# Performance work log

Hardware: AMD Instinct MI355X
Metric: run time of the kernel (lower is better)

## Reference

```python
import jax, jax.numpy as jnp
import numpy as np

D_MODEL, D_STATE, V_RANGE, IMG, K = 64, 16, 1, 32, 3
GROUPS = 4
EPS = 1e-5


def _gather_indices():
    H = W = IMG
    v_list = [(x, y) for x in range(-V_RANGE, V_RANGE + 1) for y in range(-V_RANGE, V_RANGE + 1)]
    idx = []
    yg, xg = np.meshgrid(np.arange(H), np.arange(W), indexing='ij')
    for vx, vy in v_list:
        src_y = (yg - vy) % H
        src_x = (xg - vx) % W
        idx.append((src_y * W + src_x).reshape(-1))
    return jnp.asarray(np.stack(idx, axis=0), dtype=jnp.int32)  # (V, H*W)


def setup_inputs() -> dict:
    key = jax.random.key(0)
    ks = jax.random.split(key, 8)
    B = 4
    V = (2 * V_RANGE + 1) ** 2
    fan = D_MODEL * K * K
    std = 1.0 / np.sqrt(fan)
    return {
        'u_t': jax.random.normal(ks[0], (B, D_MODEL, IMG, IMG), jnp.float32),
        's_prev': jax.random.normal(ks[1], (B, V, D_MODEL, D_STATE, IMG, IMG), jnp.float32),
        'gamma': jnp.ones((D_MODEL,), jnp.float32),
        'beta': jnp.zeros((D_MODEL,), jnp.float32),
        'w_delta': jax.random.uniform(ks[2], (D_MODEL, D_MODEL, K, K), jnp.float32, -std, std),
        'b_delta': jax.random.uniform(ks[3], (D_MODEL,), jnp.float32, -std, std),
        'w_B': jax.random.uniform(ks[4], (D_STATE, D_MODEL, K, K), jnp.float32, -std, std),
        'w_C': jax.random.uniform(ks[5], (D_STATE, D_MODEL, K, K), jnp.float32, -std, std),
        'log_A_real': jnp.log(0.5 * jnp.ones((D_MODEL, D_STATE), jnp.float32)),
        'D_param': jnp.ones((D_MODEL,), jnp.float32),
        'dt_inv_softplus': jnp.asarray(np.log(np.exp(1.0) - 1.0), jnp.float32),
        'gather_indices': _gather_indices(),
    }


def _group_norm(x, gamma, beta):
    B, D, H, W = x.shape
    xg = x.reshape(B, GROUPS, D // GROUPS, H, W)
    mu = xg.mean(axis=(2, 3, 4), keepdims=True)
    var = xg.var(axis=(2, 3, 4), keepdims=True)
    xn = ((xg - mu) / jnp.sqrt(var + EPS)).reshape(B, D, H, W)
    return xn * gamma[None, :, None, None] + beta[None, :, None, None]


def _circ_conv(x, w, b=None):
    p = K // 2
    xp = jnp.pad(x, ((0, 0), (0, 0), (p, p), (p, p)), mode='wrap')
    y = jax.lax.conv_general_dilated(xp, w, (1, 1), 'VALID',
                                     dimension_numbers=('NCHW', 'OIHW', 'NCHW'))
    if b is not None:
        y = y + b[None, :, None, None]
    return y


def reference(u_t, s_prev, gamma, beta, w_delta, b_delta, w_B, w_C,
              log_A_real, D_param, dt_inv_softplus, gather_indices):
    B, D, H, W = u_t.shape
    Bv, V, _, N, _, _ = s_prev.shape
    u_norm = _group_norm(u_t, gamma, beta)
    delta = jax.nn.softplus(_circ_conv(u_norm, w_delta, b_delta) + dt_inv_softplus)
    delta = jnp.clip(delta, 1e-4, 5.0)                      # (B,D,H,W)
    B_val = _circ_conv(u_norm, w_B)                          # (B,N,H,W)
    C_val = _circ_conv(u_norm, w_C)                          # (B,N,H,W)
    A = -jnp.exp(log_A_real)                                 # (D,N)
    A_bar = jnp.exp(delta[:, :, None] * A[None, :, :, None, None])  # (B,D,N,H,W)
    B_bar = delta[:, :, None] * B_val[:, None]               # (B,D,N,H,W)
    # flow transport: per-velocity periodic-shift gather over flattened HW
    s_flat = s_prev.reshape(B, V, D, N, H * W)
    s_trans = jax.vmap(lambda sv, iv: jnp.take(sv, iv, axis=-1),
                       in_axes=(1, 0), out_axes=1)(s_flat, gather_indices)
    s_trans = s_trans.reshape(B, V, D, N, H, W)
    s_new = A_bar[:, None] * s_trans + B_bar[:, None] * u_t[:, None, :, None]
    y_state = jnp.sum(s_new * C_val[:, None, None], axis=3)  # (B,V,D,H,W)
    y_new = y_state + u_t[:, None] * D_param[None, None, :, None, None]
    return (y_new, s_new)
```

## Files before the change

### kernel.cpp

```cpp
#include <hip/hip_runtime.h>
#include <hip/hip_bf16.h>

#define D_MODEL 64
#define D_STATE 16
#define IMG     32
#define HW      (IMG*IMG)
#define V       9
#define B       4
#define GROUPS  4
#define CPG     (D_MODEL/GROUPS)

typedef float f32x4 __attribute__((ext_vector_type(4)));

__device__ __forceinline__ void stream_store4(float* p, f32x4 v) {
    asm volatile("global_store_dwordx4 %0, %1, off sc0 sc1 nt"
                 :: "v"(p), "v"(v) : "memory");
}

__global__ __launch_bounds__(256) void gn_kernel(
    const float* __restrict__ u, const float* __restrict__ gamma,
    const float* __restrict__ beta, float* __restrict__ un)
{
    const int b = blockIdx.x / GROUPS;
    const int g = blockIdx.x % GROUPS;
    const float* base = u + ((size_t)b*D_MODEL + g*CPG) * HW;
    const int NE = CPG * HW;

    float s = 0.f, s2 = 0.f;
    for (int i = threadIdx.x; i < NE; i += 256) {
        float v = base[i];
        s += v; s2 += v*v;
    }
    for (int off = 32; off; off >>= 1) {
        s  += __shfl_down(s,  off);
        s2 += __shfl_down(s2, off);
    }
    __shared__ float red0[4], red1[4];
    const int wave = threadIdx.x >> 6;
    if ((threadIdx.x & 63) == 0) { red0[wave] = s; red1[wave] = s2; }
    __syncthreads();
    if (threadIdx.x == 0) {
        float a = 0.f, c = 0.f;
        for (int i = 0; i < 4; i++) { a += red0[i]; c += red1[i]; }
        red0[0] = a; red1[0] = c;
    }
    __syncthreads();
    const float mean = red0[0] * (1.f/16384.f);
    const float var  = red1[0] * (1.f/16384.f) - mean*mean;
    const float rstd = rsqrtf(var + 1e-5f);

    for (int i = threadIdx.x; i < NE; i += 256) {
        int c = i >> 10;
        int d = g*CPG + c;
        float v = (base[i] - mean) * rstd;
        un[((size_t)b*D_MODEL + d)*HW + (i & (HW-1))] = v*gamma[d] + beta[d];
    }
}

__global__ __launch_bounds__(256) void conv_kernel(
    const float* __restrict__ un,
    const float* __restrict__ w_delta, const float* __restrict__ b_delta,
    const float* __restrict__ w_B, const float* __restrict__ w_C,
    const float* __restrict__ dt_sp,
    float* __restrict__ delta, float* __restrict__ Bv, float* __restrict__ Cv)
{
    const int bx    = blockIdx.x;
    const int strip = bx & 3;
    const int cog   = (bx >> 2) % 24;
    const int b     = bx / 96;
    const int co0   = cog * 4;
    const int row0  = strip * 8;

    __shared__ float xs[16][10][32];
    __shared__ float wl[4][D_MODEL*9];

    for (int i = threadIdx.x; i < 4*D_MODEL*9; i += 256) {
        const int cl = i / (D_MODEL*9);
        const int rest = i % (D_MODEL*9);
        const int co = co0 + cl;
        const float* w = (co < 64) ? (w_delta + (size_t)co*(D_MODEL*9))
                       : (co < 80) ? (w_B + (size_t)(co-64)*(D_MODEL*9))
                                   : (w_C + (size_t)(co-80)*(D_MODEL*9));
        wl[cl][rest] = w[rest];
    }

    const int ly = threadIdx.x >> 5;
    const int ox = threadIdx.x & 31;
    const int oy = row0 + ly;

    const float* x = un + (size_t)b*D_MODEL*HW;
    float a0 = 0.f, a1 = 0.f, a2 = 0.f, a3 = 0.f;

    for (int c = 0; c < 4; c++) {
        __syncthreads();
        for (int i = threadIdx.x; i < 16*10*32; i += 256) {
            const int ci = i / 320;
            const int rr = (i % 320) >> 5;
            const int xx = i & 31;
            const int gy = (row0 - 1 + rr) & 31;
            xs[ci][rr][xx] = x[(size_t)(c*16 + ci)*HW + (gy << 5) + xx];
        }
        __syncthreads();

        #pragma unroll
        for (int ci = 0; ci < 16; ci++) {
            float v[3][3];
            #pragma unroll
            for (int dy = 0; dy < 3; dy++)
                #pragma unroll
                for (int dx = 0; dx < 3; dx++)
                    v[dy][dx] = xs[ci][ly + dy][(ox + dx + 31) & 31];
            const int cig = c*16 + ci;
            const float* w0 = &wl[0][cig*9];
            const float* w1 = &wl[1][cig*9];
            const float* w2 = &wl[2][cig*9];
            const float* w3 = &wl[3][cig*9];
            #pragma unroll
            for (int t = 0; t < 9; t++) {
                const float xv = v[t/3][t%3];
                a0 = fmaf(xv, w0[t], a0);
                a1 = fmaf(xv, w1[t], a1);
                a2 = fmaf(xv, w2[t], a2);
                a3 = fmaf(xv, w3[t], a3);
            }
        }
    }

    const int p = (oy << 5) + ox;
    const float dtsp = dt_sp[0];
    float accs[4] = {a0, a1, a2, a3};
    #pragma unroll
    for (int cl = 0; cl < 4; cl++) {
        const int co = co0 + cl;
        float acc = accs[cl];
        if (co < 64) {
            acc += b_delta[co] + dtsp;
            float sp = (acc > 15.f) ? acc : log1pf(__expf(acc));
            sp = fminf(fmaxf(sp, 1e-4f), 5.f);
            delta[((size_t)b*D_MODEL + co)*HW + p] = sp;
        } else if (co < 80) {
            Bv[((size_t)b*D_STATE + (co-64))*HW + p] = acc;
        } else {
            Cv[((size_t)b*D_STATE + (co-80))*HW + p] = acc;
        }
    }
}

template<int MODE>
__device__ __forceinline__ void main_body(
    const float* __restrict__ sp_base, float* __restrict__ sn_base,
    const float* __restrict__ Bv_b, const float* __restrict__ Cv_b,
    const f32x4 dl, const f32x4 du, const float* an_,
    f32x4& y, int srcv, int p0, int laneL, int laneR)
{
    #pragma unroll
    for (int n = 0; n < D_STATE; n++) {
        const f32x4 own = *(const f32x4*)(sp_base + n*HW + srcv);
        f32x4 s;
        if (MODE == 0) {
            s = own;
        } else if (MODE == 1) {
            const float nb = __shfl(own.x, laneR, 64);
            s.x = own.y; s.y = own.z; s.z = own.w; s.w = nb;
        } else {
            const float nb = __shfl(own.w, laneL, 64);
            s.x = nb; s.y = own.x; s.z = own.y; s.w = own.z;
        }
        const float anr = an_[n];
        const f32x4 Bn = *(const f32x4*)(Bv_b + n*HW);
        const f32x4 Cn = *(const f32x4*)(Cv_b + n*HW);
        f32x4 ab;
        ab.x = __expf(dl.x * anr);
        ab.y = __expf(dl.y * anr);
        ab.z = __expf(dl.z * anr);
        ab.w = __expf(dl.w * anr);
        const f32x4 sn = ab * s + du * Bn;
        stream_store4(sn_base + n*HW + p0, sn);
        y += sn * Cn;
    }
}

__global__ __launch_bounds__(256) void main_kernel(
    const float* __restrict__ sprev, const float* __restrict__ ut,
    const float* __restrict__ delta, const float* __restrict__ Bv,
    const float* __restrict__ Cv, const float* __restrict__ logA,
    const float* __restrict__ Dp, const int* __restrict__ gidx,
    float* __restrict__ ynew, float* __restrict__ snew)
{
    const int blk = blockIdx.x;
    const int d   = blk % D_MODEL;
    const int tmp = blk / D_MODEL;
    const int v   = tmp % V;
    const int b   = tmp / V;

    const int t  = threadIdx.x;
    const int p0 = t * 4;
    const int y0 = p0 >> 5;
    const int x0 = p0 & 31;

    const int gi0 = gidx[v*HW];
    const int ryo = gi0 >> 5;
    const int rxo = gi0 & 31;

    const int ys   = (y0 + ryo) & 31;
    const int srcv = (ys << 5) + x0;

    const int lane  = t & 63;
    const int laneL = (lane & ~7) | ((lane + 7) & 7);
    const int laneR = (lane & ~7) | ((lane + 1) & 7);

    const size_t bvd = (((size_t)b*V + v)*D_MODEL + d);
    const float* sp_base = sprev + bvd * D_STATE * HW;
    float* sn_base = snew + bvd * D_STATE * HW;

    const float dpd = Dp[d];
    float an_[D_STATE];
    #pragma unroll
    for (int n = 0; n < D_STATE; n++) an_[n] = -__expf(logA[d*D_STATE + n]);

    const f32x4 dl = *(const f32x4*)(delta + ((size_t)b*D_MODEL + d)*HW + p0);
    const f32x4 uu = *(const f32x4*)(ut    + ((size_t)b*D_MODEL + d)*HW + p0);
    const f32x4 du = dl * uu;
    const float* Bv_b = Bv + (size_t)b*D_STATE*HW + p0;
    const float* Cv_b = Cv + (size_t)b*D_STATE*HW + p0;

    f32x4 y = uu * dpd;

    if (rxo == 0) {
        main_body<0>(sp_base, sn_base, Bv_b, Cv_b, dl, du, an_, y, srcv, p0, laneL, laneR);
    } else if (rxo == 1) {
        main_body<1>(sp_base, sn_base, Bv_b, Cv_b, dl, du, an_, y, srcv, p0, laneL, laneR);
    } else if (rxo == 31) {
        main_body<2>(sp_base, sn_base, Bv_b, Cv_b, dl, du, an_, y, srcv, p0, laneL, laneR);
    } else {
        const int4 src4 = *(const int4*)(gidx + v*HW + p0);
        #pragma unroll
        for (int n = 0; n < D_STATE; n++) {
            const float* sp_n = sp_base + n*HW;
            const f32x4 Bn = *(const f32x4*)(Bv_b + n*HW);
            const f32x4 Cn = *(const f32x4*)(Cv_b + n*HW);
            const float anr = an_[n];
            f32x4 s;
            s.x = sp_n[src4.x]; s.y = sp_n[src4.y];
            s.z = sp_n[src4.z]; s.w = sp_n[src4.w];
            f32x4 ab;
            ab.x = __expf(dl.x * anr);
            ab.y = __expf(dl.y * anr);
            ab.z = __expf(dl.z * anr);
            ab.w = __expf(dl.w * anr);
            const f32x4 sn = ab * s + du * Bn;
            stream_store4(sn_base + n*HW + p0, sn);
            y += sn * Cn;
        }
    }
    *(f32x4*)(ynew + bvd * HW + p0) = y;
}

extern "C" void kernel_launch(void* const* d_in, const int* in_sizes, int n_in,
                              void* d_out, int out_size, void* d_ws, size_t ws_size,
                              hipStream_t stream)
{
    const float* u_t       = (const float*)d_in[0];
    const float* s_prev    = (const float*)d_in[1];
    const float* gamma     = (const float*)d_in[2];
    const float* beta      = (const float*)d_in[3];
    const float* w_delta   = (const float*)d_in[4];
    const float* b_delta   = (const float*)d_in[5];
    const float* w_B       = (const float*)d_in[6];
    const float* w_C       = (const float*)d_in[7];
    const float* log_A     = (const float*)d_in[8];
    const float* D_param   = (const float*)d_in[9];
    const float* dt_sp     = (const float*)d_in[10];
    const int*   gidx      = (const int*)d_in[11];

    float* ws = (float*)d_ws;
    float* un    = ws;
    float* delta = un    + (size_t)B*D_MODEL*HW;
    float* Bv    = delta + (size_t)B*D_MODEL*HW;
    float* Cv    = Bv    + (size_t)B*D_STATE*HW;

    float* ynew = (float*)d_out;
    float* snew = ynew + (size_t)B*V*D_MODEL*HW;

    gn_kernel<<<B*GROUPS, 256, 0, stream>>>(u_t, gamma, beta, un);
    conv_kernel<<<B*96, 256, 0, stream>>>(un, w_delta, b_delta, w_B, w_C, dt_sp,
                                          delta, Bv, Cv);
    main_kernel<<<B*V*D_MODEL, 256, 0, stream>>>(s_prev, u_t, delta, Bv, Cv,
                                                 log_A, D_param, gidx, ynew, snew);
}
```

Measured before the change: 106.8 us.

## Software-pipeline state loads with inline asm and explicit vmcnt waits

Replaces the unrolled per-state loop in the shifted-copy paths with a manually pipelined body. It issues raw global_load_dwordx4 instructions four state slices ahead and uses hand-tuned s_waitcnt vmcnt values with scheduling barriers, so loads of s_prev, B and C overlap with the compute and stores. The inline-asm streaming store is also replaced by the compiler's nontemporal store builtin. The hand-counted vmcnt values assume a specific mix of outstanding loads and stores. That is fragile if the compiler reorders or adds memory operations, and the nontemporal builtin may emit different cache-policy bits than the old sc0 sc1 nt store.

```diff
diff --git a/kernel.cpp b/kernel.cpp
--- a/kernel.cpp
+++ b/kernel.cpp
@@ -11,11 +11,6 @@
 #define CPG     (D_MODEL/GROUPS)
 
 typedef float f32x4 __attribute__((ext_vector_type(4)));
-
-__device__ __forceinline__ void stream_store4(float* p, f32x4 v) {
-    asm volatile("global_store_dwordx4 %0, %1, off sc0 sc1 nt"
-                 :: "v"(p), "v"(v) : "memory");
-}
 
 __global__ __launch_bounds__(256) void gn_kernel(
     const float* __restrict__ u, const float* __restrict__ gamma,
@@ -146,38 +141,58 @@
     }
 }
 
+__device__ __forceinline__ f32x4 asm_load4(const float* __restrict__ base, unsigned voff) {
+    f32x4 d;
+    asm volatile("global_load_dwordx4 %0, %1, %2"
+                 : "=v"(d) : "v"(voff), "s"(base) : "memory");
+    return d;
+}
+
+#define STEP(n, K) do { \
+    if ((n) + 4 <= 15) { \
+        sp[((n)+4)&15] = asm_load4(sp_u, sp_voff + ((n)+4)*4096u); \
+        Bn[((n)+4)&15] = asm_load4(Bv_u, bc_voff + ((n)+4)*4096u); \
+        Cn[((n)+4)&15] = asm_load4(Cv_u, bc_voff + ((n)+4)*4096u); \
+    } \
+    asm volatile("s_waitcnt vmcnt(" #K ")" ::: "memory"); \
+    __builtin_amdgcn_sched_barrier(0); \
+    { \
+        const f32x4 own = sp[(n)]; \
+        f32x4 s; \
+        if (MODE == 0) { s = own; } \
+        else if (MODE == 1) { const float nb = __shfl(own.x, laneR, 64); \
+                              s.x = own.y; s.y = own.z; s.z = own.w; s.w = nb; } \
+        else { const float nb = __shfl(own.w, laneL, 64); \
+               s.x = nb; s.y = own.x; s.z = own.y; s.w = own.z; } \
+        const float anr = an_[(n)]; \
+        f32x4 ab; \
+        ab.x = __expf(dl.x*anr); ab.y = __expf(dl.y*anr); \
+        ab.z = __expf(dl.z*anr); ab.w = __expf(dl.w*anr); \
+        const f32x4 snv = ab*s + du*Bn[(n)]; \
+        __builtin_nontemporal_store(snv, (f32x4*)(sn_p + (n)*HW)); \
+        y += snv * Cn[(n)]; \
+    } \
+} while (0)
+
 template<int MODE>
-__device__ __forceinline__ void main_body(
-    const float* __restrict__ sp_base, float* __restrict__ sn_base,
-    const float* __restrict__ Bv_b, const float* __restrict__ Cv_b,
+__device__ __forceinline__ void pipe_body(
+    const float* __restrict__ sp_u, unsigned sp_voff,
+    const float* __restrict__ Bv_u, const float* __restrict__ Cv_u, unsigned bc_voff,
+    float* __restrict__ sn_p,
     const f32x4 dl, const f32x4 du, const float* an_,
-    f32x4& y, int srcv, int p0, int laneL, int laneR)
-{
+    f32x4& y, int laneL, int laneR)
+{
+    f32x4 sp[16], Bn[16], Cn[16];
     #pragma unroll
-    for (int n = 0; n < D_STATE; n++) {
-        const f32x4 own = *(const f32x4*)(sp_base + n*HW + srcv);
-        f32x4 s;
-        if (MODE == 0) {
-            s = own;
-        } else if (MODE == 1) {
-            const float nb = __shfl(own.x, laneR, 64);
-            s.x = own.y; s.y = own.z; s.z = own.w; s.w = nb;
-        } else {
-            const float nb = __shfl(own.w, laneL, 64);
-            s.x = nb; s.y = own.x; s.z = own.y; s.w = own.z;
-        }
-        const float anr = an_[n];
-        const f32x4 Bn = *(const f32x4*)(Bv_b + n*HW);
-        const f32x4 Cn = *(const f32x4*)(Cv_b + n*HW);
-        f32x4 ab;
-        ab.x = __expf(dl.x * anr);
-        ab.y = __expf(dl.y * anr);
-        ab.z = __expf(dl.z * anr);
-        ab.w = __expf(dl.w * anr);
-        const f32x4 sn = ab * s + du * Bn;
-        stream_store4(sn_base + n*HW + p0, sn);
-        y += sn * Cn;
-    }
+    for (int p = 0; p < 4; p++) {
+        sp[p] = asm_load4(sp_u, sp_voff + p*4096u);
+        Bn[p] = asm_load4(Bv_u, bc_voff + p*4096u);
+        Cn[p] = asm_load4(Cv_u, bc_voff + p*4096u);
+    }
+    STEP(0, 12); STEP(1, 13); STEP(2, 14); STEP(3, 15);
+    STEP(4, 16); STEP(5, 16); STEP(6, 16); STEP(7, 16);
+    STEP(8, 16); STEP(9, 16); STEP(10, 16); STEP(11, 16);
+    STEP(12, 13); STEP(13, 10); STEP(14, 7); STEP(15, 4);
 }
 
 __global__ __launch_bounds__(256) void main_kernel(
@@ -210,8 +225,8 @@
     const int laneR = (lane & ~7) | ((lane + 1) & 7);
 
     const size_t bvd = (((size_t)b*V + v)*D_MODEL + d);
-    const float* sp_base = sprev + bvd * D_STATE * HW;
-    float* sn_base = snew + bvd * D_STATE * HW;
+    const float* sp_u = sprev + bvd * D_STATE * HW;
+    float* sn_p = snew + bvd * D_STATE * HW + p0;
 
     const float dpd = Dp[d];
     float an_[D_STATE];
@@ -221,24 +236,27 @@
     const f32x4 dl = *(const f32x4*)(delta + ((size_t)b*D_MODEL + d)*HW + p0);
     const f32x4 uu = *(const f32x4*)(ut    + ((size_t)b*D_MODEL + d)*HW + p0);
     const f32x4 du = dl * uu;
-    const float* Bv_b = Bv + (size_t)b*D_STATE*HW + p0;
-    const float* Cv_b = Cv + (size_t)b*D_STATE*HW + p0;
+    const float* Bv_u = Bv + (size_t)b*D_STATE*HW;
+    const float* Cv_u = Cv + (size_t)b*D_STATE*HW;
 
     f32x4 y = uu * dpd;
 
+    const unsigned sp_voff = (unsigned)srcv * 4u;
+    const unsigned bc_voff = (unsigned)p0 * 4u;
+
     if (rxo == 0) {
-        main_body<0>(sp_base, sn_base, Bv_b, Cv_b, dl, du, an_, y, srcv, p0, laneL, laneR);
+        pipe_body<0>(sp_u, sp_voff, Bv_u, Cv_u, bc_voff, sn_p, dl, du, an_, y, laneL, laneR);
     } else if (rxo == 1) {
-        main_body<1>(sp_base, sn_base, Bv_b, Cv_b, dl, du, an_, y, srcv, p0, laneL, laneR);
+        pipe_body<1>(sp_u, sp_voff, Bv_u, Cv_u, bc_voff, sn_p, dl, du, an_, y, laneL, laneR);
     } else if (rxo == 31) {
-        main_body<2>(sp_base, sn_base, Bv_b, Cv_b, dl, du, an_, y, srcv, p0, laneL, laneR);
+        pipe_body<2>(sp_u, sp_voff, Bv_u, Cv_u, bc_voff, sn_p, dl, du, an_, y, laneL, laneR);
     } else {
         const int4 src4 = *(const int4*)(gidx + v*HW + p0);
         #pragma unroll
         for (int n = 0; n < D_STATE; n++) {
-            const float* sp_n = sp_base + n*HW;
-            const f32x4 Bn = *(const f32x4*)(Bv_b + n*HW);
-            const f32x4 Cn = *(const f32x4*)(Cv_b + n*HW);
+            const float* sp_n = sp_u + n*HW;
+            const f32x4 Bn = *(const f32x4*)(Bv_u + n*HW + p0);
+            const f32x4 Cn = *(const f32x4*)(Cv_u + n*HW + p0);
             const float anr = an_[n];
             f32x4 s;
             s.x = sp_n[src4.x]; s.y = sp_n[src4.y];
@@ -249,7 +267,7 @@
             ab.z = __expf(dl.z * anr);
             ab.w = __expf(dl.w * anr);
             const f32x4 sn = ab * s + du * Bn;
-            stream_store4(sn_base + n*HW + p0, sn);
+            __builtin_nontemporal_store(sn, (f32x4*)(sn_p + n*HW));
             y += sn * Cn;
         }
     }
```

After: 102.4 us. 4.1% less time.
